# Kernel tuning notes

Measured on AMD Instinct MI355X. Metric: run time of the kernel, lower is better.

The kernel has to match this reference:

```python
import math
import jax, jax.numpy as jnp
import numpy as np

G = 128        # graphs per batch
N0 = 512       # nodes per graph
H = 256        # hidden size
E = 524288     # edges (avg degree 8), intra-graph
RATIO = 0.8


def setup_inputs() -> dict:
    key = jax.random.key(0)
    ks = jax.random.split(key, 16)
    # intra-graph edges: E//G edges per graph
    eg = jnp.arange(E, dtype=jnp.int32) // (E // G)
    src = eg * N0 + jax.random.randint(ks[0], (E,), 0, N0, dtype=jnp.int32)
    dst = eg * N0 + jax.random.randint(ks[1], (E,), 0, N0, dtype=jnp.int32)
    s = 1.0 / math.sqrt(H)
    return {
        "x": jax.random.normal(ks[2], (G * N0, H), jnp.float32),
        "edge_src": src,
        "edge_dst": dst,
        "W_in": jax.random.normal(ks[3], (H, H), jnp.float32) * s,
        "b_in": jnp.zeros((H,), jnp.float32),
        "W_h0": jax.random.normal(ks[4], (H, H), jnp.float32) * s,
        "b_h0": jnp.zeros((H,), jnp.float32),
        "W_h1": jax.random.normal(ks[5], (H, H), jnp.float32) * s,
        "b_h1": jnp.zeros((H,), jnp.float32),
        "p_in": jax.random.normal(ks[6], (H,), jnp.float32),
        "p_h0": jax.random.normal(ks[7], (H,), jnp.float32),
        "p_h1": jax.random.normal(ks[8], (H,), jnp.float32),
        "att_w": jax.random.normal(ks[9], (H,), jnp.float32) * s,
        "att_b": jnp.zeros((1,), jnp.float32),
    }


def gcn_conv(x, W, b, src, dst, emask, num_nodes):
    # PyG GCNConv: lin -> sym-normalized propagate (with self loops, weight 1) -> bias
    h = x @ W
    deg = jax.ops.segment_sum(emask, dst, num_segments=num_nodes) + 1.0  # +1 self loop
    dis = jax.lax.rsqrt(deg)
    coef = dis[src] * dis[dst] * emask                    # [E]
    agg = jax.ops.segment_sum(h[src] * coef[:, None], dst, num_segments=num_nodes)
    agg = agg + h * (dis * dis)[:, None]                  # self-loop message
    return agg + b


def topk_pool(x, p, src, dst, emask, n_cur):
    # PyG TopKPooling: score = tanh(x.p/|p|), keep top ceil(ratio*n) per graph,
    # x' = x[perm]*score[perm], edges filtered to kept nodes and remapped.
    k = int(math.ceil(RATIO * n_cur))
    score = jnp.tanh((x @ p) / jnp.linalg.norm(p))        # [G*n_cur]
    _, idx = jax.lax.top_k(score.reshape(G, n_cur), k)    # [G,k]
    perm = (idx + (jnp.arange(G, dtype=idx.dtype) * n_cur)[:, None]).reshape(-1)
    x_new = x[perm] * score[perm][:, None]                # [G*k,H]
    mapping = jnp.full((G * n_cur,), -1, jnp.int32).at[perm].set(
        jnp.arange(G * k, dtype=jnp.int32))
    ns, nd = mapping[src], mapping[dst]
    valid = (ns >= 0) & (nd >= 0) & (emask > 0)
    return (x_new, jnp.where(valid, ns, 0), jnp.where(valid, nd, 0),
            valid.astype(x.dtype), k)


def att_pool(x, att_w, att_b, k):
    # GlobalAttention: per-graph softmax gate, weighted sum
    gate = (x @ att_w + att_b[0]).reshape(G, k)
    att = jax.nn.softmax(gate, axis=1)
    return jnp.einsum('gk,gkh->gh', att, x.reshape(G, k, H))


def reference(x, edge_src, edge_dst, W_in, b_in, W_h0, b_h0, W_h1, b_h1,
              p_in, p_h0, p_h1, att_w, att_b):
    src, dst = edge_src, edge_dst
    emask = jnp.ones((E,), x.dtype)
    n_cur = N0
    h = jax.nn.relu(gcn_conv(x, W_in, b_in, src, dst, emask, G * n_cur))
    h, src, dst, emask, n_cur = topk_pool(h, p_in, src, dst, emask, n_cur)
    out = att_pool(h, att_w, att_b, n_cur)
    for (W, b, p) in ((W_h0, b_h0, p_h0), (W_h1, b_h1, p_h1)):
        h = jax.nn.relu(gcn_conv(h, W, b, src, dst, emask, G * n_cur))
        h, src, dst, emask, n_cur = topk_pool(h, p, src, dst, emask, n_cur)
        out = out + att_pool(h, att_w, att_b, n_cur)
    return out  # [G, H]
```

## Files before the change

### kernel.cpp

```cpp
#include <hip/hip_runtime.h>
#include <cmath>

#define G_ 128
#define N0_ 512
#define H_ 256
#define E_ 524288
#define NODES0 (G_*N0_)

typedef _Float16 v8h __attribute__((ext_vector_type(8)));
typedef _Float16 v4h __attribute__((ext_vector_type(4)));
typedef float v4f __attribute__((ext_vector_type(4)));

#define TSTRIDE 72

__device__ __forceinline__ void async_copy16(void* lds, const void* g) {
  __builtin_amdgcn_global_load_lds(
      (const __attribute__((address_space(1))) void*)g,
      (__attribute__((address_space(3))) void*)lds, 16, 0, 0);
}

__device__ __forceinline__ float4 f4fma(float4 a, float s, float4 acc) {
  acc.x = fmaf(a.x, s, acc.x); acc.y = fmaf(a.y, s, acc.y);
  acc.z = fmaf(a.z, s, acc.z); acc.w = fmaf(a.w, s, acc.w);
  return acc;
}

__device__ __forceinline__ float block_reduce_sum(float v, volatile float* red) {
  #pragma unroll
  for (int off = 32; off > 0; off >>= 1) v += __shfl_down(v, off);
  int lane = threadIdx.x & 63, wid = threadIdx.x >> 6;
  __syncthreads();
  if (lane == 0) red[wid] = v;
  __syncthreads();
  return red[0] + red[1] + red[2] + red[3];
}

__global__ __launch_bounds__(256) void pnorm_kernel(const float* __restrict__ p0,
                                                    const float* __restrict__ p1,
                                                    const float* __restrict__ p2,
                                                    float* __restrict__ pinv) {
  __shared__ float red[4];
  const float* p = (blockIdx.x == 0) ? p0 : (blockIdx.x == 1 ? p1 : p2);
  float v = p[threadIdx.x];
  float s = block_reduce_sum(v * v, red);
  if (threadIdx.x == 0) pinv[blockIdx.x] = 1.0f / sqrtf(s);
}

__global__ void init_cum_kernel(int* __restrict__ cum, int n) {
  int v = blockIdx.x * 256 + threadIdx.x;
  if (v < n) cum[v] = v;
}

__global__ __launch_bounds__(256) void wconv_kernel(const float* __restrict__ W,
                                                    _Float16* __restrict__ img) {
  int bn = blockIdx.x >> 3, kt = blockIdx.x & 7;
  int t = threadIdx.x;
  int n = t & 127, kh = t >> 7;
  int k0 = kt * 32 + kh * 16;
  _Float16* row = img + ((size_t)(bn * 8 + kt) * 128 + n) * TSTRIDE;
  #pragma unroll
  for (int s = 0; s < 2; ++s) {
    v8h hv, lv;
    #pragma unroll
    for (int j = 0; j < 8; ++j) {
      float a = W[(size_t)(k0 + s * 8 + j) * 256 + bn * 128 + n];
      _Float16 h = (_Float16)a;
      hv[j] = h;
      lv[j] = (_Float16)(a - (float)h);
    }
    *(v8h*)&row[kh * 16 + s * 8] = hv;
    *(v8h*)&row[32 + kh * 16 + s * 8] = lv;
  }
}

__global__ __launch_bounds__(256) void gemm_f16x3_kernel(const float* __restrict__ A,
                                                         const _Float16* __restrict__ Wimg,
                                                         float* __restrict__ C) {
  __shared__ _Float16 As[128 * TSTRIDE];
  __shared__ _Float16 Ws[128 * TSTRIDE];
  const int tid = threadIdx.x;
  const int bm = blockIdx.x >> 1;
  const int bn = blockIdx.x & 1;
  const int lane = tid & 63, wid = tid >> 6;
  const int wm = wid >> 1, wn = wid & 1;
  const int l15 = lane & 15, kg = lane >> 4;

  v4f acc[4][4];
  #pragma unroll
  for (int i = 0; i < 4; ++i)
    #pragma unroll
    for (int j = 0; j < 4; ++j) acc[i][j] = (v4f){0.f, 0.f, 0.f, 0.f};

  int arow[4], acc4[4];
  const float* aptr[4];
  #pragma unroll
  for (int i = 0; i < 4; ++i) {
    int c = tid + 256 * i;
    arow[i] = c >> 3;
    acc4[i] = c & 7;
    aptr[i] = A + (size_t)(bm * 128 + arow[i]) * 256 + acc4[i] * 4;
  }
  const _Float16* wtile0 = Wimg + (size_t)bn * 8 * 128 * TSTRIDE;

  float4 pa[4];
  #pragma unroll
  for (int i = 0; i < 4; ++i) pa[i] = *(const float4*)(aptr[i] + 0);

  for (int kt = 0; kt < 8; ++kt) {
    {
      const _Float16* wt = wtile0 + (size_t)kt * 128 * TSTRIDE;
      for (int cb = wid; cb < 18; cb += 4)
        async_copy16(&Ws[cb * 512 + 0], wt + (size_t)cb * 512 + lane * 8);
    }
    #pragma unroll
    for (int i = 0; i < 4; ++i) {
      float av[4] = {pa[i].x, pa[i].y, pa[i].z, pa[i].w};
      v4h hv, lv;
      #pragma unroll
      for (int j = 0; j < 4; ++j) {
        _Float16 h = (_Float16)av[j];
        hv[j] = h;
        lv[j] = (_Float16)(av[j] - (float)h);
      }
      _Float16* dst = &As[arow[i] * TSTRIDE + acc4[i] * 4];
      *(v4h*)(dst) = hv;
      *(v4h*)(dst + 32) = lv;
    }
    __syncthreads();

    if (kt < 7) {
      #pragma unroll
      for (int i = 0; i < 4; ++i)
        pa[i] = *(const float4*)(aptr[i] + (kt + 1) * 32);
    }

    v8h ah[4], bh[4], al[4], bl[4];
    #pragma unroll
    for (int i = 0; i < 4; ++i)
      ah[i] = *(const v8h*)&As[(wm * 64 + i * 16 + l15) * TSTRIDE + kg * 8];
    #pragma unroll
    for (int j = 0; j < 4; ++j)
      bh[j] = *(const v8h*)&Ws[(wn * 64 + j * 16 + l15) * TSTRIDE + kg * 8];
    #pragma unroll
    for (int i = 0; i < 4; ++i)
      #pragma unroll
      for (int j = 0; j < 4; ++j)
        acc[i][j] = __builtin_amdgcn_mfma_f32_16x16x32_f16(ah[i], bh[j], acc[i][j], 0, 0, 0);
    #pragma unroll
    for (int i = 0; i < 4; ++i)
      al[i] = *(const v8h*)&As[(wm * 64 + i * 16 + l15) * TSTRIDE + 32 + kg * 8];
    #pragma unroll
    for (int i = 0; i < 4; ++i)
      #pragma unroll
      for (int j = 0; j < 4; ++j)
        acc[i][j] = __builtin_amdgcn_mfma_f32_16x16x32_f16(al[i], bh[j], acc[i][j], 0, 0, 0);
    #pragma unroll
    for (int j = 0; j < 4; ++j)
      bl[j] = *(const v8h*)&Ws[(wn * 64 + j * 16 + l15) * TSTRIDE + 32 + kg * 8];
    #pragma unroll
    for (int i = 0; i < 4; ++i)
      #pragma unroll
      for (int j = 0; j < 4; ++j)
        acc[i][j] = __builtin_amdgcn_mfma_f32_16x16x32_f16(ah[i], bl[j], acc[i][j], 0, 0, 0);
    __syncthreads();
  }

  #pragma unroll
  for (int i = 0; i < 4; ++i) {
    #pragma unroll
    for (int j = 0; j < 4; ++j) {
      #pragma unroll
      for (int r = 0; r < 4; ++r) {
        int row = bm * 128 + wm * 64 + i * 16 + kg * 4 + r;
        int col = bn * 128 + wn * 64 + j * 16 + l15;
        C[(size_t)row * 256 + col] = acc[i][j][r];
      }
    }
  }
}

__global__ void count_deg_kernel(const int* __restrict__ esrc, const int* __restrict__ edst,
                                 const int* __restrict__ cum, int* __restrict__ cnt) {
  int e = blockIdx.x * 256 + threadIdx.x;
  if (e >= E_) return;
  int ms = cum[esrc[e]], md = cum[edst[e]];
  if (ms >= 0 && md >= 0) atomicAdd(&cnt[md], 1);
}

__global__ __launch_bounds__(256) void scan1_kernel(const int* __restrict__ cnt,
                                                    int* __restrict__ row_start,
                                                    int* __restrict__ bsum,
                                                    float* __restrict__ dis, int n) {
  __shared__ int sdata[256];
  int base = blockIdx.x * 1024;
  int t = threadIdx.x;
  int v[4]; int s = 0;
  #pragma unroll
  for (int i = 0; i < 4; ++i) {
    int idx = base + t * 4 + i;
    v[i] = (idx < n) ? cnt[idx] : 0;
    s += v[i];
    if (idx < n) dis[idx] = 1.0f / sqrtf((float)v[i] + 1.0f);
  }
  sdata[t] = s;
  __syncthreads();
  for (int off = 1; off < 256; off <<= 1) {
    int x = (t >= off) ? sdata[t - off] : 0;
    __syncthreads();
    sdata[t] += x;
    __syncthreads();
  }
  int excl = sdata[t] - s;
  if (t == 255) bsum[blockIdx.x] = sdata[255];
  #pragma unroll
  for (int i = 0; i < 4; ++i) {
    int idx = base + t * 4 + i;
    if (idx < n) { row_start[idx] = excl; excl += v[i]; }
  }
}

__global__ __launch_bounds__(256) void scan2_kernel(int* __restrict__ bsum,
                                                    int* __restrict__ row_start, int nb, int n) {
  __shared__ int sdata[256];
  int t = threadIdx.x;
  int v = (t < nb) ? bsum[t] : 0;
  sdata[t] = v;
  __syncthreads();
  for (int off = 1; off < 256; off <<= 1) {
    int x = (t >= off) ? sdata[t - off] : 0;
    __syncthreads();
    sdata[t] += x;
    __syncthreads();
  }
  if (t < nb) bsum[t] = sdata[t] - v;
  if (t == 255) row_start[n] = sdata[255];
}

__global__ void scan3_kernel(int* __restrict__ row_start, const int* __restrict__ bsum, int n) {
  int idx = blockIdx.x * 256 + threadIdx.x;
  if (idx < n) row_start[idx] += bsum[idx >> 10];
}

__global__ void fill_csr_kernel(const int* __restrict__ esrc, const int* __restrict__ edst,
                                const int* __restrict__ cum, const int* __restrict__ row_start,
                                int* __restrict__ cursor, const float* __restrict__ dis,
                                int* __restrict__ csr_src, float* __restrict__ csr_cf) {
  int e = blockIdx.x * 256 + threadIdx.x;
  if (e >= E_) return;
  int ms = cum[esrc[e]], md = cum[edst[e]];
  if (ms < 0 || md < 0) return;
  int pos = atomicAdd(&cursor[md], 1);
  int j = row_start[md] + pos;
  csr_src[j] = ms;
  csr_cf[j] = dis[ms] * dis[md];
}

__global__ __launch_bounds__(256) void agg_score_kernel(
    const float4* __restrict__ hlin4, const float* __restrict__ dis,
    const float4* __restrict__ bias4,
    const int* __restrict__ row_start, const int* __restrict__ csr_src,
    const float* __restrict__ csr_cf, const float4* __restrict__ p4,
    const float* __restrict__ pinvp,
    float4* __restrict__ hout4, float* __restrict__ score, int q) {
  int blk = (blockIdx.x & 7) * q + (blockIdx.x >> 3);
  int wave = threadIdx.x >> 6, lane = threadIdx.x & 63;
  int v = blk * 4 + wave;
  float dv = dis[v];
  float self = dv * dv;
  float4 h = hlin4[(size_t)v * 64 + lane];
  float4 acc = make_float4(h.x * self, h.y * self, h.z * self, h.w * self);
  int rs = row_start[v], re = row_start[v + 1];
  int j = rs;
  for (; j + 4 <= re; j += 4) {
    int s0 = csr_src[j + 0], s1 = csr_src[j + 1];
    int s2 = csr_src[j + 2], s3 = csr_src[j + 3];
    float c0 = csr_cf[j + 0], c1 = csr_cf[j + 1];
    float c2 = csr_cf[j + 2], c3 = csr_cf[j + 3];
    float4 h0 = hlin4[(size_t)s0 * 64 + lane];
    float4 h1 = hlin4[(size_t)s1 * 64 + lane];
    float4 h2 = hlin4[(size_t)s2 * 64 + lane];
    float4 h3 = hlin4[(size_t)s3 * 64 + lane];
    acc = f4fma(h0, c0, acc); acc = f4fma(h1, c1, acc);
    acc = f4fma(h2, c2, acc); acc = f4fma(h3, c3, acc);
  }
  for (; j < re; ++j) {
    acc = f4fma(hlin4[(size_t)csr_src[j] * 64 + lane], csr_cf[j], acc);
  }
  float4 b = bias4[lane];
  acc.x = fmaxf(acc.x + b.x, 0.0f); acc.y = fmaxf(acc.y + b.y, 0.0f);
  acc.z = fmaxf(acc.z + b.z, 0.0f); acc.w = fmaxf(acc.w + b.w, 0.0f);
  hout4[(size_t)v * 64 + lane] = acc;
  float4 pv = p4[lane];
  float s = acc.x * pv.x + acc.y * pv.y + acc.z * pv.z + acc.w * pv.w;
  #pragma unroll
  for (int off = 32; off > 0; off >>= 1) s += __shfl_down(s, off);
  if (lane == 0) score[v] = tanhf(s * pinvp[0]);
}

__global__ __launch_bounds__(256) void topk_kernel(const float* __restrict__ score, int n, int k,
                                                   int* __restrict__ cur_map, int* __restrict__ perm) {
  __shared__ float key[512];
  __shared__ int kid[512];
  int g = blockIdx.x, t = threadIdx.x;
  for (int i = t; i < 512; i += 256) {
    key[i] = (i < n) ? score[(size_t)g * n + i] : -INFINITY;
    kid[i] = i;
  }
  for (int i = t; i < n; i += 256) cur_map[g * n + i] = -1;
  __syncthreads();
  for (int kk = 2; kk <= 512; kk <<= 1) {
    for (int j = kk >> 1; j > 0; j >>= 1) {
      #pragma unroll
      for (int half = 0; half < 2; ++half) {
        int i = t + half * 256;
        int ixj = i ^ j;
        if (ixj > i) {
          float ka = key[i]; int ia = kid[i];
          float kb = key[ixj]; int ib = kid[ixj];
          bool b_first = (kb > ka) || (kb == ka && ib < ia);
          bool sw = ((i & kk) == 0) ? b_first : !b_first;
          if (sw) { key[i] = kb; kid[i] = ib; key[ixj] = ka; kid[ixj] = ia; }
        }
      }
      __syncthreads();
    }
  }
  for (int i = t; i < k; i += 256) {
    int local = kid[i];
    perm[g * k + i] = g * n + local;
    cur_map[g * n + local] = g * k + i;
  }
}

__global__ void update_cum_kernel(int* __restrict__ cum, const int* __restrict__ cur_map, int n0) {
  int v = blockIdx.x * 256 + threadIdx.x;
  if (v < n0) {
    int c = cum[v];
    if (c >= 0) cum[v] = cur_map[c];
  }
}

__global__ __launch_bounds__(256) void gather_gate_kernel(
    const float4* __restrict__ h4, const float* __restrict__ score, const int* __restrict__ perm,
    const float4* __restrict__ attw4, const float* __restrict__ attb,
    float4* __restrict__ xnew4, float* __restrict__ gate, int q) {
  int blk = (blockIdx.x & 7) * q + (blockIdx.x >> 3);
  int wave = threadIdx.x >> 6, lane = threadIdx.x & 63;
  int i = blk * 4 + wave;
  int s = perm[i];
  float sc = score[s];
  float4 h = h4[(size_t)s * 64 + lane];
  float4 val = make_float4(h.x * sc, h.y * sc, h.z * sc, h.w * sc);
  xnew4[(size_t)i * 64 + lane] = val;
  float4 aw = attw4[lane];
  float g = val.x * aw.x + val.y * aw.y + val.z * aw.z + val.w * aw.w;
  #pragma unroll
  for (int off = 32; off > 0; off >>= 1) g += __shfl_down(g, off);
  if (lane == 0) gate[i] = g + attb[0];
}

__global__ __launch_bounds__(512) void att_pool_kernel(const float4* __restrict__ x4,
                                                       const float* __restrict__ gate,
                                                       float* __restrict__ out, int k, int add) {
  __shared__ float att[512];
  __shared__ float red[8];
  __shared__ float4 part[512];
  int g = blockIdx.x, t = threadIdx.x;
  int wave = t >> 6, lane = t & 63;
  const float* gg = gate + (size_t)g * k;

  float m = -INFINITY;
  for (int i = t; i < k; i += 512) m = fmaxf(m, gg[i]);
  #pragma unroll
  for (int off = 32; off > 0; off >>= 1) m = fmaxf(m, __shfl_down(m, off));
  if (lane == 0) red[wave] = m;
  __syncthreads();
  m = red[0];
  #pragma unroll
  for (int w = 1; w < 8; ++w) m = fmaxf(m, red[w]);
  __syncthreads();

  float s = 0.0f;
  for (int i = t; i < k; i += 512) {
    float e = expf(gg[i] - m);
    att[i] = e;
    s += e;
  }
  #pragma unroll
  for (int off = 32; off > 0; off >>= 1) s += __shfl_down(s, off);
  if (lane == 0) red[wave] = s;
  __syncthreads();
  s = red[0] + red[1] + red[2] + red[3] + red[4] + red[5] + red[6] + red[7];
  float inv = 1.0f / s;

  float4 acc = make_float4(0.f, 0.f, 0.f, 0.f);
  const float4* xg = x4 + (size_t)g * k * 64;
  for (int i = wave; i < k; i += 8) acc = f4fma(xg[(size_t)i * 64 + lane], att[i], acc);
  part[t] = acc;
  __syncthreads();
  if (wave == 0) {
    float4 r = part[lane];
    #pragma unroll
    for (int w = 1; w < 8; ++w) {
      float4 pw = part[w * 64 + lane];
      r.x += pw.x; r.y += pw.y; r.z += pw.z; r.w += pw.w;
    }
    r.x *= inv; r.y *= inv; r.z *= inv; r.w *= inv;
    float4* o4 = (float4*)out + (size_t)g * 64 + lane;
    if (add) {
      float4 prev = *o4;
      r.x += prev.x; r.y += prev.y; r.z += prev.z; r.w += prev.w;
    }
    *o4 = r;
  }
}

extern "C" void kernel_launch(void* const* d_in, const int* in_sizes, int n_in,
                              void* d_out, int out_size, void* d_ws, size_t ws_size,
                              hipStream_t stream) {
  const float* x    = (const float*)d_in[0];
  const int*   esrc = (const int*)d_in[1];
  const int*   edst = (const int*)d_in[2];
  const float* Wl[3] = {(const float*)d_in[3], (const float*)d_in[5], (const float*)d_in[7]};
  const float* bl[3] = {(const float*)d_in[4], (const float*)d_in[6], (const float*)d_in[8]};
  const float* pl[3] = {(const float*)d_in[9], (const float*)d_in[10], (const float*)d_in[11]};
  const float* attw = (const float*)d_in[12];
  const float* attb = (const float*)d_in[13];
  float* out = (float*)d_out;

  char* w = (char*)d_ws;
  auto carve = [&](size_t bytes) { char* p = w; w += (bytes + 255) & ~(size_t)255; return p; };
  float* bufA    = (float*)carve((size_t)NODES0 * H_ * 4);
  float* bufB    = (float*)carve((size_t)NODES0 * H_ * 4);
  int*   csr_src = (int*)  carve((size_t)E_ * 4);
  float* csr_cf  = (float*)carve((size_t)E_ * 4);
  int*   cnt     = (int*)  carve((size_t)NODES0 * 4);
  int*   row_st  = (int*)  carve((size_t)(NODES0 + 1) * 4);
  int*   cursor  = (int*)  carve((size_t)NODES0 * 4);
  float* dis     = (float*)carve((size_t)NODES0 * 4);
  float* score   = (float*)carve((size_t)NODES0 * 4);
  int*   cur_map = (int*)  carve((size_t)NODES0 * 4);
  int*   cum_map = (int*)  carve((size_t)NODES0 * 4);
  int*   perm    = (int*)  carve((size_t)NODES0 * 4);
  float* gate    = (float*)carve((size_t)NODES0 * 4);
  int*   bsum    = (int*)  carve(256 * 4);
  float* pinv    = (float*)carve(16);
  _Float16* Wimg = (_Float16*)carve((size_t)2 * 8 * 128 * TSTRIDE * 2);
  (void)ws_size; (void)in_sizes; (void)n_in; (void)out_size;

  pnorm_kernel<<<3, 256, 0, stream>>>(pl[0], pl[1], pl[2], pinv);
  init_cum_kernel<<<NODES0 / 256, 256, 0, stream>>>(cum_map, NODES0);

  int n_cur = N0_;
  const float* xin = x;
  for (int l = 0; l < 3; ++l) {
    int nodes = G_ * n_cur;
    float* hlin = (l & 1) ? bufB : bufA;
    float* hbuf = (l & 1) ? bufA : bufB;
    float* xnew = hlin;

    wconv_kernel<<<16, 256, 0, stream>>>(Wl[l], Wimg);
    gemm_f16x3_kernel<<<(nodes / 128) * 2, 256, 0, stream>>>(xin, Wimg, hlin);

    hipMemsetAsync(cnt, 0, (size_t)nodes * 4, stream);
    count_deg_kernel<<<E_ / 256, 256, 0, stream>>>(esrc, edst, cum_map, cnt);
    int nb = (nodes + 1023) / 1024;
    scan1_kernel<<<nb, 256, 0, stream>>>(cnt, row_st, bsum, dis, nodes);
    scan2_kernel<<<1, 256, 0, stream>>>(bsum, row_st, nb, nodes);
    scan3_kernel<<<(nodes + 255) / 256, 256, 0, stream>>>(row_st, bsum, nodes);
    hipMemsetAsync(cursor, 0, (size_t)nodes * 4, stream);
    fill_csr_kernel<<<E_ / 256, 256, 0, stream>>>(esrc, edst, cum_map, row_st, cursor, dis,
                                                  csr_src, csr_cf);

    int agg_blocks = nodes / 4;
    agg_score_kernel<<<agg_blocks, 256, 0, stream>>>(
        (const float4*)hlin, dis, (const float4*)bl[l], row_st, csr_src, csr_cf,
        (const float4*)pl[l], pinv + l, (float4*)hbuf, score, agg_blocks / 8);

    int kk = (int)std::ceil(0.8 * (double)n_cur);
    topk_kernel<<<G_, 256, 0, stream>>>(score, n_cur, kk, cur_map, perm);
    update_cum_kernel<<<NODES0 / 256, 256, 0, stream>>>(cum_map, cur_map, NODES0);
    int rows = G_ * kk;
    int gg_blocks = rows / 4;
    gather_gate_kernel<<<gg_blocks, 256, 0, stream>>>(
        (const float4*)hbuf, score, perm, (const float4*)attw, attb,
        (float4*)xnew, gate, gg_blocks / 8);

    att_pool_kernel<<<G_, 512, 0, stream>>>((const float4*)xnew, gate, out, kk, l > 0 ? 1 : 0);

    n_cur = kk;
    xin = xnew;
  }
}
```

Measured before the change: 447.3 us.

## Cut launches, double-buffer GEMM tiles, and unroll aggregation gathers

Converts all three weight matrices in one launch up front instead of one per layer. Folds the cnt and cursor memsets into existing kernels, and merges the cum_map update into topk through an LDS map. The GEMM now double-buffers its A and W LDS tiles so the next tile loads while the current one computes. The aggregation loop gathers eight neighbours per iteration for more memory-level parallelism, at the cost of more LDS and registers, which may lower occupancy.

```diff
diff --git a/kernel.cpp b/kernel.cpp
--- a/kernel.cpp
+++ b/kernel.cpp
@@ -12,6 +12,7 @@
 typedef float v4f __attribute__((ext_vector_type(4)));
 
 #define TSTRIDE 72
+#define TILEHW (128*TSTRIDE)
 
 __device__ __forceinline__ void async_copy16(void* lds, const void* g) {
   __builtin_amdgcn_global_load_lds(
@@ -46,18 +47,22 @@
   if (threadIdx.x == 0) pinv[blockIdx.x] = 1.0f / sqrtf(s);
 }
 
-__global__ void init_cum_kernel(int* __restrict__ cum, int n) {
+__global__ void init_cum_kernel(int* __restrict__ cum, int* __restrict__ cnt, int n) {
   int v = blockIdx.x * 256 + threadIdx.x;
-  if (v < n) cum[v] = v;
-}
-
-__global__ __launch_bounds__(256) void wconv_kernel(const float* __restrict__ W,
+  if (v < n) { cum[v] = v; cnt[v] = 0; }
+}
+
+__global__ __launch_bounds__(256) void wconv_kernel(const float* __restrict__ W0,
+                                                    const float* __restrict__ W1,
+                                                    const float* __restrict__ W2,
                                                     _Float16* __restrict__ img) {
-  int bn = blockIdx.x >> 3, kt = blockIdx.x & 7;
+  int l = blockIdx.x >> 4;
+  const float* W = (l == 0) ? W0 : (l == 1 ? W1 : W2);
+  int bn = (blockIdx.x >> 3) & 1, kt = blockIdx.x & 7;
   int t = threadIdx.x;
   int n = t & 127, kh = t >> 7;
   int k0 = kt * 32 + kh * 16;
-  _Float16* row = img + ((size_t)(bn * 8 + kt) * 128 + n) * TSTRIDE;
+  _Float16* row = img + (size_t)l * 16 * TILEHW + ((size_t)(bn * 8 + kt) * 128 + n) * TSTRIDE;
   #pragma unroll
   for (int s = 0; s < 2; ++s) {
     v8h hv, lv;
@@ -76,8 +81,8 @@
 __global__ __launch_bounds__(256) void gemm_f16x3_kernel(const float* __restrict__ A,
                                                          const _Float16* __restrict__ Wimg,
                                                          float* __restrict__ C) {
-  __shared__ _Float16 As[128 * TSTRIDE];
-  __shared__ _Float16 Ws[128 * TSTRIDE];
+  __shared__ _Float16 As[2][TILEHW];
+  __shared__ _Float16 Ws[2][TILEHW];
   const int tid = threadIdx.x;
   const int bm = blockIdx.x >> 1;
   const int bn = blockIdx.x & 1;
@@ -100,18 +105,19 @@
     acc4[i] = c & 7;
     aptr[i] = A + (size_t)(bm * 128 + arow[i]) * 256 + acc4[i] * 4;
   }
-  const _Float16* wtile0 = Wimg + (size_t)bn * 8 * 128 * TSTRIDE;
+  const _Float16* wtile0 = Wimg + (size_t)bn * 8 * TILEHW;
 
   float4 pa[4];
-  #pragma unroll
-  for (int i = 0; i < 4; ++i) pa[i] = *(const float4*)(aptr[i] + 0);
-
-  for (int kt = 0; kt < 8; ++kt) {
-    {
-      const _Float16* wt = wtile0 + (size_t)kt * 128 * TSTRIDE;
-      for (int cb = wid; cb < 18; cb += 4)
-        async_copy16(&Ws[cb * 512 + 0], wt + (size_t)cb * 512 + lane * 8);
-    }
+
+  auto issueW = [&](int kt, int buf) {
+    const _Float16* wt = wtile0 + (size_t)kt * TILEHW;
+    #pragma unroll
+    for (int cb = 0; cb < 5; ++cb) {
+      int c = wid + cb * 4;
+      if (c < 18) async_copy16(&Ws[buf][c * 512], wt + (size_t)c * 512 + lane * 8);
+    }
+  };
+  auto convertA = [&](int buf) {
     #pragma unroll
     for (int i = 0; i < 4; ++i) {
       float av[4] = {pa[i].x, pa[i].y, pa[i].z, pa[i].w};
@@ -122,25 +128,36 @@
         hv[j] = h;
         lv[j] = (_Float16)(av[j] - (float)h);
       }
-      _Float16* dst = &As[arow[i] * TSTRIDE + acc4[i] * 4];
+      _Float16* dst = &As[buf][arow[i] * TSTRIDE + acc4[i] * 4];
       *(v4h*)(dst) = hv;
       *(v4h*)(dst + 32) = lv;
     }
-    __syncthreads();
-
+  };
+  auto loadA = [&](int kt) {
+    #pragma unroll
+    for (int i = 0; i < 4; ++i) pa[i] = *(const float4*)(aptr[i] + kt * 32);
+  };
+
+  loadA(0);
+  issueW(0, 0);
+  convertA(0);
+  loadA(1);
+  __syncthreads();
+
+  for (int kt = 0; kt < 8; ++kt) {
+    int cur = kt & 1;
     if (kt < 7) {
-      #pragma unroll
-      for (int i = 0; i < 4; ++i)
-        pa[i] = *(const float4*)(aptr[i] + (kt + 1) * 32);
-    }
-
+      issueW(kt + 1, cur ^ 1);
+      convertA(cur ^ 1);
+      if (kt < 6) loadA(kt + 2);
+    }
     v8h ah[4], bh[4], al[4], bl[4];
     #pragma unroll
     for (int i = 0; i < 4; ++i)
-      ah[i] = *(const v8h*)&As[(wm * 64 + i * 16 + l15) * TSTRIDE + kg * 8];
+      ah[i] = *(const v8h*)&As[cur][(wm * 64 + i * 16 + l15) * TSTRIDE + kg * 8];
     #pragma unroll
     for (int j = 0; j < 4; ++j)
-      bh[j] = *(const v8h*)&Ws[(wn * 64 + j * 16 + l15) * TSTRIDE + kg * 8];
+      bh[j] = *(const v8h*)&Ws[cur][(wn * 64 + j * 16 + l15) * TSTRIDE + kg * 8];
     #pragma unroll
     for (int i = 0; i < 4; ++i)
       #pragma unroll
@@ -148,7 +165,7 @@
         acc[i][j] = __builtin_amdgcn_mfma_f32_16x16x32_f16(ah[i], bh[j], acc[i][j], 0, 0, 0);
     #pragma unroll
     for (int i = 0; i < 4; ++i)
-      al[i] = *(const v8h*)&As[(wm * 64 + i * 16 + l15) * TSTRIDE + 32 + kg * 8];
+      al[i] = *(const v8h*)&As[cur][(wm * 64 + i * 16 + l15) * TSTRIDE + 32 + kg * 8];
     #pragma unroll
     for (int i = 0; i < 4; ++i)
       #pragma unroll
@@ -156,13 +173,13 @@
         acc[i][j] = __builtin_amdgcn_mfma_f32_16x16x32_f16(al[i], bh[j], acc[i][j], 0, 0, 0);
     #pragma unroll
     for (int j = 0; j < 4; ++j)
-      bl[j] = *(const v8h*)&Ws[(wn * 64 + j * 16 + l15) * TSTRIDE + 32 + kg * 8];
+      bl[j] = *(const v8h*)&Ws[cur][(wn * 64 + j * 16 + l15) * TSTRIDE + 32 + kg * 8];
     #pragma unroll
     for (int i = 0; i < 4; ++i)
       #pragma unroll
       for (int j = 0; j < 4; ++j)
         acc[i][j] = __builtin_amdgcn_mfma_f32_16x16x32_f16(ah[i], bl[j], acc[i][j], 0, 0, 0);
-    __syncthreads();
+    if (kt < 7) __syncthreads();
   }
 
   #pragma unroll
@@ -190,7 +207,8 @@
 __global__ __launch_bounds__(256) void scan1_kernel(const int* __restrict__ cnt,
                                                     int* __restrict__ row_start,
                                                     int* __restrict__ bsum,
-                                                    float* __restrict__ dis, int n) {
+                                                    float* __restrict__ dis,
+                                                    int* __restrict__ cursor, int n) {
   __shared__ int sdata[256];
   int base = blockIdx.x * 1024;
   int t = threadIdx.x;
@@ -200,7 +218,10 @@
     int idx = base + t * 4 + i;
     v[i] = (idx < n) ? cnt[idx] : 0;
     s += v[i];
-    if (idx < n) dis[idx] = 1.0f / sqrtf((float)v[i] + 1.0f);
+    if (idx < n) {
+      dis[idx] = 1.0f / sqrtf((float)v[i] + 1.0f);
+      cursor[idx] = 0;
+    }
   }
   sdata[t] = s;
   __syncthreads();
@@ -236,9 +257,10 @@
   if (t == 255) row_start[n] = sdata[255];
 }
 
-__global__ void scan3_kernel(int* __restrict__ row_start, const int* __restrict__ bsum, int n) {
+__global__ void scan3_kernel(int* __restrict__ row_start, const int* __restrict__ bsum,
+                             int* __restrict__ cnt, int n) {
   int idx = blockIdx.x * 256 + threadIdx.x;
-  if (idx < n) row_start[idx] += bsum[idx >> 10];
+  if (idx < n) { row_start[idx] += bsum[idx >> 10]; cnt[idx] = 0; }
 }
 
 __global__ void fill_csr_kernel(const int* __restrict__ esrc, const int* __restrict__ edst,
@@ -271,17 +293,24 @@
   float4 acc = make_float4(h.x * self, h.y * self, h.z * self, h.w * self);
   int rs = row_start[v], re = row_start[v + 1];
   int j = rs;
-  for (; j + 4 <= re; j += 4) {
-    int s0 = csr_src[j + 0], s1 = csr_src[j + 1];
-    int s2 = csr_src[j + 2], s3 = csr_src[j + 3];
-    float c0 = csr_cf[j + 0], c1 = csr_cf[j + 1];
-    float c2 = csr_cf[j + 2], c3 = csr_cf[j + 3];
-    float4 h0 = hlin4[(size_t)s0 * 64 + lane];
-    float4 h1 = hlin4[(size_t)s1 * 64 + lane];
-    float4 h2 = hlin4[(size_t)s2 * 64 + lane];
-    float4 h3 = hlin4[(size_t)s3 * 64 + lane];
-    acc = f4fma(h0, c0, acc); acc = f4fma(h1, c1, acc);
-    acc = f4fma(h2, c2, acc); acc = f4fma(h3, c3, acc);
+  for (; j + 8 <= re; j += 8) {
+    int s[8]; float c[8]; float4 hh[8];
+    #pragma unroll
+    for (int u = 0; u < 8; ++u) { s[u] = csr_src[j + u]; c[u] = csr_cf[j + u]; }
+    #pragma unroll
+    for (int u = 0; u < 8; ++u) hh[u] = hlin4[(size_t)s[u] * 64 + lane];
+    #pragma unroll
+    for (int u = 0; u < 8; ++u) acc = f4fma(hh[u], c[u], acc);
+  }
+  if (j + 4 <= re) {
+    int s[4]; float c[4]; float4 hh[4];
+    #pragma unroll
+    for (int u = 0; u < 4; ++u) { s[u] = csr_src[j + u]; c[u] = csr_cf[j + u]; }
+    #pragma unroll
+    for (int u = 0; u < 4; ++u) hh[u] = hlin4[(size_t)s[u] * 64 + lane];
+    #pragma unroll
+    for (int u = 0; u < 4; ++u) acc = f4fma(hh[u], c[u], acc);
+    j += 4;
   }
   for (; j < re; ++j) {
     acc = f4fma(hlin4[(size_t)csr_src[j] * 64 + lane], csr_cf[j], acc);
@@ -298,15 +327,16 @@
 }
 
 __global__ __launch_bounds__(256) void topk_kernel(const float* __restrict__ score, int n, int k,
-                                                   int* __restrict__ cur_map, int* __restrict__ perm) {
+                                                   int* __restrict__ cum, int* __restrict__ perm) {
   __shared__ float key[512];
   __shared__ int kid[512];
+  __shared__ int newmap[512];
   int g = blockIdx.x, t = threadIdx.x;
   for (int i = t; i < 512; i += 256) {
     key[i] = (i < n) ? score[(size_t)g * n + i] : -INFINITY;
     kid[i] = i;
-  }
-  for (int i = t; i < n; i += 256) cur_map[g * n + i] = -1;
+    if (i < n) newmap[i] = -1;
+  }
   __syncthreads();
   for (int kk = 2; kk <= 512; kk <<= 1) {
     for (int j = kk >> 1; j > 0; j >>= 1) {
@@ -328,15 +358,14 @@
   for (int i = t; i < k; i += 256) {
     int local = kid[i];
     perm[g * k + i] = g * n + local;
-    cur_map[g * n + local] = g * k + i;
-  }
-}
-
-__global__ void update_cum_kernel(int* __restrict__ cum, const int* __restrict__ cur_map, int n0) {
-  int v = blockIdx.x * 256 + threadIdx.x;
-  if (v < n0) {
+    newmap[local] = g * k + i;
+  }
+  __syncthreads();
+  #pragma unroll
+  for (int u = 0; u < N0_ / 256; ++u) {
+    int v = g * N0_ + u * 256 + t;
     int c = cum[v];
-    if (c >= 0) cum[v] = cur_map[c];
+    if (c >= 0) cum[v] = newmap[c - g * n];
   }
 }
 
@@ -439,17 +468,17 @@
   int*   cursor  = (int*)  carve((size_t)NODES0 * 4);
   float* dis     = (float*)carve((size_t)NODES0 * 4);
   float* score   = (float*)carve((size_t)NODES0 * 4);
-  int*   cur_map = (int*)  carve((size_t)NODES0 * 4);
   int*   cum_map = (int*)  carve((size_t)NODES0 * 4);
   int*   perm    = (int*)  carve((size_t)NODES0 * 4);
   float* gate    = (float*)carve((size_t)NODES0 * 4);
   int*   bsum    = (int*)  carve(256 * 4);
   float* pinv    = (float*)carve(16);
-  _Float16* Wimg = (_Float16*)carve((size_t)2 * 8 * 128 * TSTRIDE * 2);
+  _Float16* Wimg = (_Float16*)carve((size_t)3 * 16 * TILEHW * 2);
   (void)ws_size; (void)in_sizes; (void)n_in; (void)out_size;
 
   pnorm_kernel<<<3, 256, 0, stream>>>(pl[0], pl[1], pl[2], pinv);
-  init_cum_kernel<<<NODES0 / 256, 256, 0, stream>>>(cum_map, NODES0);
+  init_cum_kernel<<<NODES0 / 256, 256, 0, stream>>>(cum_map, cnt, NODES0);
+  wconv_kernel<<<48, 256, 0, stream>>>(Wl[0], Wl[1], Wl[2], Wimg);
 
   int n_cur = N0_;
   const float* xin = x;
@@ -459,16 +488,14 @@
     float* hbuf = (l & 1) ? bufA : bufB;
     float* xnew = hlin;
 
-    wconv_kernel<<<16, 256, 0, stream>>>(Wl[l], Wimg);
-    gemm_f16x3_kernel<<<(nodes / 128) * 2, 256, 0, stream>>>(xin, Wimg, hlin);
-
-    hipMemsetAsync(cnt, 0, (size_t)nodes * 4, stream);
+    gemm_f16x3_kernel<<<(nodes / 128) * 2, 256, 0, stream>>>(
+        xin, Wimg + (size_t)l * 16 * TILEHW, hlin);
+
     count_deg_kernel<<<E_ / 256, 256, 0, stream>>>(esrc, edst, cum_map, cnt);
     int nb = (nodes + 1023) / 1024;
-    scan1_kernel<<<nb, 256, 0, stream>>>(cnt, row_st, bsum, dis, nodes);
+    scan1_kernel<<<nb, 256, 0, stream>>>(cnt, row_st, bsum, dis, cursor, nodes);
     scan2_kernel<<<1, 256, 0, stream>>>(bsum, row_st, nb, nodes);
-    scan3_kernel<<<(nodes + 255) / 256, 256, 0, stream>>>(row_st, bsum, nodes);
-    hipMemsetAsync(cursor, 0, (size_t)nodes * 4, stream);
+    scan3_kernel<<<(nodes + 255) / 256, 256, 0, stream>>>(row_st, bsum, cnt, nodes);
     fill_csr_kernel<<<E_ / 256, 256, 0, stream>>>(esrc, edst, cum_map, row_st, cursor, dis,
                                                   csr_src, csr_cf);
 
@@ -478,8 +505,7 @@
         (const float4*)pl[l], pinv + l, (float4*)hbuf, score, agg_blocks / 8);
 
     int kk = (int)std::ceil(0.8 * (double)n_cur);
-    topk_kernel<<<G_, 256, 0, stream>>>(score, n_cur, kk, cur_map, perm);
-    update_cum_kernel<<<NODES0 / 256, 256, 0, stream>>>(cum_map, cur_map, NODES0);
+    topk_kernel<<<G_, 256, 0, stream>>>(score, n_cur, kk, cum_map, perm);
     int rows = G_ * kk;
     int gg_blocks = rows / 4;
     gather_gate_kernel<<<gg_blocks, 256, 0, stream>>>(
```

New measurement: 449.6 us. About the same (+0.5%).
